# Optimization experiments

Measured on AMD Instinct MI355X. Metric: run time of the kernel, lower is better.

The kernel has to match this reference:

```python
import jax, jax.numpy as jnp
import numpy as np
from jax import lax

C = 32    # feats_channels
CT = 16   # transform_channels
B, D, H, W = 1, 16, 16, 32  # N = D*H*W = 8192


def _bcast(v):
    return v[None, :, None, None, None]


def conv1(x, w):
    # 1x1x1 Conv3d, no bias: w [O, I], x [b, I, d, h, w]
    return jnp.einsum('oi,bidhw->bodhw', w, x)


def cbr(x, w, s, b):
    # Conv1x1x1 + inference BatchNorm (folded to scale s / bias b) + ReLU
    return jax.nn.relu(conv1(x, w) * _bcast(s) + _bcast(b))


def setup_inputs() -> dict:
    key = jax.random.key(0)
    ks = jax.random.split(key, 16)

    def wmat(k, shape, scale=0.05):
        return jax.random.normal(k, shape, jnp.float32) * scale

    def bn(k, n):
        k1, k2 = jax.random.split(k)
        s = 1.0 + 0.05 * jax.random.normal(k1, (n,), jnp.float32)
        b = 0.05 * jax.random.normal(k2, (n,), jnp.float32)
        return s, b

    inp = {'x': jax.random.normal(ks[0], (B, C, D, H, W), jnp.float32)}
    # query_project: 2 convs (C->CT, CT->CT), each conv+BN+ReLU
    inp['wq1'] = wmat(ks[1], (CT, C));  inp['sq1'], inp['bq1'] = bn(ks[2], CT)
    inp['wq2'] = wmat(ks[3], (CT, CT)); inp['sq2'], inp['bq2'] = bn(ks[4], CT)
    # key_project: 2 convs (2C->CT, CT->CT)
    inp['wk1'] = wmat(ks[5], (CT, 2 * C)); inp['sk1'], inp['bk1'] = bn(ks[6], CT)
    inp['wk2'] = wmat(ks[7], (CT, CT));    inp['sk2'], inp['bk2'] = bn(ks[8], CT)
    # value_project: 1 conv (2C->CT) + BN + ReLU
    inp['wv'] = wmat(ks[9], (CT, 2 * C)); inp['sv'], inp['bv'] = bn(ks[10], CT)
    # out_project: 1 conv (CT->C) + BN + ReLU
    inp['wo'] = wmat(ks[11], (C, CT)); inp['so'], inp['bo'] = bn(ks[12], C)
    # bottleneck: Conv3d(2C->C, k=3, pad=1, no bias) + BN + LeakyReLU(0.1)
    inp['wbot'] = wmat(ks[13], (C, 2 * C, 3, 3, 3), 0.02)
    inp['sbot'], inp['bbot'] = bn(ks[14], C)
    return inp


def reference(x, wq1, sq1, bq1, wq2, sq2, bq2,
              wk1, sk1, bk1, wk2, sk2, bk2,
              wv, sv, bv, wo, so, bo, wbot, sbot, bbot):
    b, c, d, h, w = x.shape
    # AdaptiveAvgPool2d((1,1)) on (b, c*d, h, w) = mean over (h, w) per (c,d);
    # bilinear upsample from 1x1 is a constant broadcast.
    xg = jnp.mean(x, axis=(3, 4), keepdims=True)
    key_feats = jnp.concatenate([jnp.broadcast_to(xg, x.shape), x], axis=1)  # [b, 2c, d, h, w]

    q = cbr(cbr(x, wq1, sq1, bq1), wq2, sq2, bq2)          # [b, CT, d, h, w]
    k = cbr(cbr(key_feats, wk1, sk1, bk1), wk2, sk2, bk2)  # [b, CT, d, h, w]
    v = cbr(key_feats, wv, sv, bv)                          # [b, CT, d, h, w]

    n = d * h * w
    q = q.reshape(b, CT, n).transpose(0, 2, 1)  # [b, N, CT]
    k = k.reshape(b, CT, n)                     # [b, CT, N]
    v = v.reshape(b, CT, n).transpose(0, 2, 1)  # [b, N, CT]

    sim = jnp.einsum('bnc,bcm->bnm', q, k) * (CT ** -0.5)   # [b, N, N]
    sim = jax.nn.softmax(sim, axis=-1)
    ctx = jnp.einsum('bnm,bmc->bnc', sim, v)                # [b, N, CT]
    ctx = ctx.transpose(0, 2, 1).reshape(b, CT, d, h, w)
    ctx = cbr(ctx, wo, so, bo)                              # [b, C, d, h, w]

    fused = jnp.concatenate([x, ctx], axis=1)               # [b, 2C, d, h, w]
    y = lax.conv_general_dilated(
        fused, wbot, window_strides=(1, 1, 1), padding='SAME',
        dimension_numbers=('NCDHW', 'OIDHW', 'NCDHW'))
    y = y * _bcast(sbot) + _bcast(bbot)
    return jnp.where(y > 0, y, 0.1 * y)  # LeakyReLU(0.1)
```

## Files before the change

### kernel.cpp

```cpp
#include <hip/hip_runtime.h>

typedef unsigned int u32;
typedef unsigned short u16;
typedef float f32x16 __attribute__((ext_vector_type(16)));
typedef __bf16 bf16x8 __attribute__((ext_vector_type(8)));
union BF8 { u32 w[4]; bf16x8 v; };

#define DEVI static __device__ __forceinline__
DEVI u32 pk_bf16(float lo, float hi) {
  u32 r;
  asm("v_cvt_pk_bf16_f32 %0, %1, %2" : "=v"(r) : "v"(lo), "v"(hi));
  return r;
}
DEVI u16 bf1(float x) { return (u16)(pk_bf16(x, 0.0f) & 0xffffu); }

#define WB_WREP  0
#define WB_QS    131072
#define WB_K     393216
#define WB_VT    655360
#define WB_FUS   917504

__global__ __launch_bounds__(256) void k_prep(
    const float* __restrict__ x,
    const float* __restrict__ wq1, const float* __restrict__ sq1, const float* __restrict__ bq1,
    const float* __restrict__ wq2, const float* __restrict__ sq2, const float* __restrict__ bq2,
    const float* __restrict__ wk1, const float* __restrict__ sk1, const float* __restrict__ bk1,
    const float* __restrict__ wk2, const float* __restrict__ sk2, const float* __restrict__ bk2,
    const float* __restrict__ wv,  const float* __restrict__ sv,  const float* __restrict__ bv,
    const float* __restrict__ wbot, const float* __restrict__ sbot,
    u16* __restrict__ qs, u16* __restrict__ kbm, u16* __restrict__ vt,
    u16* __restrict__ fus, u16* __restrict__ wrep) {
  const int tid = threadIdx.x;
  const int bid = blockIdx.x;
  if (bid >= 256) {
    const int rb = bid - 256;
#pragma unroll
    for (int e = 0; e < 8; ++e) {
      const int idx = rb * 2048 + tid * 8 + e;
      const int tap = idx >> 11, rem = idx & 2047, o = rem >> 6, i = rem & 63;
      wrep[idx] = bf1(wbot[(o * 64 + i) * 27 + tap] * sbot[o]);
    }
    return;
  }
  __shared__ float H[2][32][17];
  __shared__ float P8[32][8];
  __shared__ float xgs[32];
  const int n0 = bid << 5;
  const int d = n0 >> 9;
  {
    const int c = tid >> 3, part = tid & 7;
    const float4* xp = (const float4*)(x + (c << 13) + (d << 9));
    float s = 0.f;
#pragma unroll
    for (int i = 0; i < 16; ++i) {
      const float4 v4 = xp[part + (i << 3)];
      s += v4.x + v4.y + v4.z + v4.w;
    }
    P8[c][part] = s;
  }
  __syncthreads();
  if (tid < 32) {
    float s = 0.f;
#pragma unroll
    for (int j = 0; j < 8; ++j) s += P8[tid][j];
    xgs[tid] = s * (1.0f / 512.0f);
  }
  __syncthreads();
  const int nl = tid & 31, g = tid >> 5;
  const int n = n0 + nl;
  const int r0 = 2 * g, r1 = r0 + 1;
  float xr[32], xgv[32];
#pragma unroll
  for (int c = 0; c < 32; ++c) xr[c] = x[(c << 13) + n];
#pragma unroll
  for (int c = 0; c < 32; ++c) xgv[c] = xgs[c];

  const float4* wq1f = (const float4*)wq1;
  const float4* wk1f = (const float4*)wk1;
  const float4* wvf  = (const float4*)wv;
  float dq0 = 0.f, dq1 = 0.f, dk0 = 0.f, dk1 = 0.f, dv0 = 0.f, dv1 = 0.f;
#pragma unroll
  for (int c4 = 0; c4 < 8; ++c4) {
    const float4 wa = wq1f[r0 * 8 + c4], wb = wq1f[r1 * 8 + c4];
    dq0 += wa.x * xr[4*c4+0] + wa.y * xr[4*c4+1] + wa.z * xr[4*c4+2] + wa.w * xr[4*c4+3];
    dq1 += wb.x * xr[4*c4+0] + wb.y * xr[4*c4+1] + wb.z * xr[4*c4+2] + wb.w * xr[4*c4+3];
  }
#pragma unroll
  for (int c4 = 0; c4 < 8; ++c4) {
    const float4 ka = wk1f[r0 * 16 + c4], kb = wk1f[r1 * 16 + c4];
    dk0 += ka.x * xgv[4*c4+0] + ka.y * xgv[4*c4+1] + ka.z * xgv[4*c4+2] + ka.w * xgv[4*c4+3];
    dk1 += kb.x * xgv[4*c4+0] + kb.y * xgv[4*c4+1] + kb.z * xgv[4*c4+2] + kb.w * xgv[4*c4+3];
    const float4 va = wvf[r0 * 16 + c4], vb = wvf[r1 * 16 + c4];
    dv0 += va.x * xgv[4*c4+0] + va.y * xgv[4*c4+1] + va.z * xgv[4*c4+2] + va.w * xgv[4*c4+3];
    dv1 += vb.x * xgv[4*c4+0] + vb.y * xgv[4*c4+1] + vb.z * xgv[4*c4+2] + vb.w * xgv[4*c4+3];
  }
#pragma unroll
  for (int c4 = 0; c4 < 8; ++c4) {
    const float4 ka = wk1f[r0 * 16 + 8 + c4], kb = wk1f[r1 * 16 + 8 + c4];
    dk0 += ka.x * xr[4*c4+0] + ka.y * xr[4*c4+1] + ka.z * xr[4*c4+2] + ka.w * xr[4*c4+3];
    dk1 += kb.x * xr[4*c4+0] + kb.y * xr[4*c4+1] + kb.z * xr[4*c4+2] + kb.w * xr[4*c4+3];
    const float4 va = wvf[r0 * 16 + 8 + c4], vb = wvf[r1 * 16 + 8 + c4];
    dv0 += va.x * xr[4*c4+0] + va.y * xr[4*c4+1] + va.z * xr[4*c4+2] + va.w * xr[4*c4+3];
    dv1 += vb.x * xr[4*c4+0] + vb.y * xr[4*c4+1] + vb.z * xr[4*c4+2] + vb.w * xr[4*c4+3];
  }
  const float hq0 = fmaxf(dq0 * sq1[r0] + bq1[r0], 0.f);
  const float hq1 = fmaxf(dq1 * sq1[r1] + bq1[r1], 0.f);
  const float hk0 = fmaxf(dk0 * sk1[r0] + bk1[r0], 0.f);
  const float hk1 = fmaxf(dk1 * sk1[r1] + bk1[r1], 0.f);
  const float hv0 = fmaxf(dv0 * sv[r0] + bv[r0], 0.f);
  const float hv1 = fmaxf(dv1 * sv[r1] + bv[r1], 0.f);
  H[0][nl][r0] = hq0; H[0][nl][r1] = hq1;
  H[1][nl][r0] = hk0; H[1][nl][r1] = hk1;
  vt[(r0 << 13) + n] = bf1(hv0);
  vt[(r1 << 13) + n] = bf1(hv1);
  const int c0 = g << 2;
  *(u32*)(fus + (n << 6) + c0)     = pk_bf16(xr[c0],     xr[c0 + 1]);
  *(u32*)(fus + (n << 6) + c0 + 2) = pk_bf16(xr[c0 + 2], xr[c0 + 3]);
  __syncthreads();

  float eq0 = 0.f, eq1 = 0.f, ek0 = 0.f, ek1 = 0.f;
#pragma unroll
  for (int j = 0; j < 16; ++j) {
    const float hq = H[0][nl][j], hk = H[1][nl][j];
    eq0 += wq2[r0 * 16 + j] * hq;
    eq1 += wq2[r1 * 16 + j] * hq;
    ek0 += wk2[r0 * 16 + j] * hk;
    ek1 += wk2[r1 * 16 + j] * hk;
  }
  const float SC = 0.36067376022224085f;
  const float q0 = fmaxf(eq0 * (sq2[r0] * SC) + bq2[r0] * SC, 0.f);
  const float q1 = fmaxf(eq1 * (sq2[r1] * SC) + bq2[r1] * SC, 0.f);
  const float k0 = fmaxf(ek0 * sk2[r0] + bk2[r0], 0.f);
  const float k1 = fmaxf(ek1 * sk2[r1] + bk2[r1], 0.f);
  *(u32*)(qs  + (n << 4) + r0) = pk_bf16(q0, q1);
  *(u32*)(kbm + (n << 4) + r0) = pk_bf16(k0, k1);
}

__global__ __launch_bounds__(1024) void k_attn(
    const u16* __restrict__ qs, const u16* __restrict__ kbm, const u16* __restrict__ vt,
    const float* __restrict__ wo, const float* __restrict__ so, const float* __restrict__ bo,
    u16* __restrict__ fus) {
  __shared__ float R[16][32][17];
  const int tid = threadIdx.x;
  const int w = tid >> 6, lane = tid & 63;
  const int l31 = lane & 31, h = lane >> 5;
  const int qb = blockIdx.x;

  const bf16x8 qf = *(const bf16x8*)(qs + (((qb << 5) + l31) << 4) + (h << 3));
  f32x16 acc_a, acc_b, z;
#pragma unroll
  for (int i = 0; i < 16; ++i) { acc_a[i] = 0.f; acc_b[i] = 0.f; z[i] = 0.f; }

  const u32 fill = (l31 == 16) ? 0x3F803F80u : 0u;
  const int kb0 = w << 9;
  const bool vlane = (l31 < 16);
  const u16* vrow = vt + (l31 << 13) + (h << 3);

  bf16x8 kf_c = *(const bf16x8*)(kbm + ((kb0 + l31) << 4) + (h << 3));
  BF8 V1c, V2c;
#pragma unroll
  for (int j2 = 0; j2 < 4; ++j2) { V1c.w[j2] = fill; V2c.w[j2] = fill; }
  if (vlane) {
    V1c.v = *(const bf16x8*)(vrow + kb0);
    V2c.v = *(const bf16x8*)(vrow + kb0 + 16);
  }

#pragma unroll
  for (int t = 0; t < 16; ++t) {
    const bf16x8 kf = kf_c;
    const BF8 V1 = V1c, V2 = V2c;
    if (t < 15) {
      const int kbn = kb0 + ((t + 1) << 5);
      kf_c = *(const bf16x8*)(kbm + ((kbn + l31) << 4) + (h << 3));
      if (vlane) {
        V1c.v = *(const bf16x8*)(vrow + kbn);
        V2c.v = *(const bf16x8*)(vrow + kbn + 16);
      }
    }
    const f32x16 st = __builtin_amdgcn_mfma_f32_32x32x16_bf16(kf, qf, z, 0, 0, 0);
    float pe[16];
#pragma unroll
    for (int r = 0; r < 16; ++r) pe[r] = __builtin_amdgcn_exp2f(st[r]);
    u32 a0 = pk_bf16(pe[0],  pe[1]),  a1 = pk_bf16(pe[2],  pe[3]);
    u32 a2 = pk_bf16(pe[4],  pe[5]),  a3 = pk_bf16(pe[6],  pe[7]);
    u32 b0 = pk_bf16(pe[8],  pe[9]),  b1 = pk_bf16(pe[10], pe[11]);
    u32 b2 = pk_bf16(pe[12], pe[13]), b3 = pk_bf16(pe[14], pe[15]);
    asm("v_permlane32_swap_b32 %0, %1" : "+v"(a0), "+v"(a2));
    asm("v_permlane32_swap_b32 %0, %1" : "+v"(a1), "+v"(a3));
    asm("v_permlane32_swap_b32 %0, %1" : "+v"(b0), "+v"(b2));
    asm("v_permlane32_swap_b32 %0, %1" : "+v"(b1), "+v"(b3));
    BF8 A1, A2;
    A1.w[0] = a0; A1.w[1] = a1; A1.w[2] = a2; A1.w[3] = a3;
    A2.w[0] = b0; A2.w[1] = b1; A2.w[2] = b2; A2.w[3] = b3;
    __builtin_amdgcn_s_setprio(1);
    acc_a = __builtin_amdgcn_mfma_f32_32x32x16_bf16(A1.v, V1.v, acc_a, 0, 0, 0);
    acc_b = __builtin_amdgcn_mfma_f32_32x32x16_bf16(A2.v, V2.v, acc_b, 0, 0, 0);
    __builtin_amdgcn_s_setprio(0);
  }
  if (l31 < 17) {
#pragma unroll
    for (int r = 0; r < 16; ++r) {
      const int row = (r & 3) + ((r >> 2) << 3) + (h << 2);
      R[w][row][l31] = acc_a[r] + acc_b[r];
    }
  }
  __syncthreads();
  float* Rf = &R[0][0][0];
  if (tid < 544) {
    float s0 = 0.f;
#pragma unroll
    for (int w2 = 0; w2 < 16; ++w2) s0 += Rf[w2 * 544 + tid];
    Rf[tid] = s0;
  }
  __syncthreads();
  if (tid < 512) {
    const int row = tid >> 4;
    const int o0 = (tid & 15) << 1, o1 = o0 + 1;
    const float inv = 1.0f / Rf[row * 17 + 16];
    float d0 = 0.f, d1 = 0.f;
#pragma unroll
    for (int c = 0; c < 16; ++c) {
      const float cv = Rf[row * 17 + c];
      d0 += wo[o0 * 16 + c] * cv;
      d1 += wo[o1 * 16 + c] * cv;
    }
    const float y0 = fmaxf(bo[o0] + so[o0] * d0 * inv, 0.f);
    const float y1 = fmaxf(bo[o1] + so[o1] * d1 * inv, 0.f);
    *(u32*)(fus + (((qb << 5) + row) << 6) + 32 + o0) = pk_bf16(y0, y1);
  }
}

__global__ __launch_bounds__(512) void k_conv(
    const u16* __restrict__ fus, const u16* __restrict__ wrep,
    const float* __restrict__ bbot, float* __restrict__ out) {
  __shared__ float R8[8][1024];
  const int tid = threadIdx.x;
  const int wv = tid >> 6, lane = tid & 63;
  const int l31 = lane & 31, h = lane >> 5;
  const int n0 = blockIdx.x << 5;
  const int dz = n0 >> 9, hy = (n0 >> 5) & 15;
  f32x16 acc0, acc1;
#pragma unroll
  for (int i = 0; i < 16; ++i) { acc0[i] = 0.f; acc1[i] = 0.f; }
  const int ulo = (wv * 54) >> 3, uhi = ((wv + 1) * 54) >> 3;

  const u16* bp_c; const u16* wp_c; bool ok_c;
  {
    const int tap = ulo >> 1, ch = (ulo & 1) << 1;
    const int dd = tap / 9 - 1, dh = (tap / 3) % 3 - 1, dw = tap % 3 - 1;
    ok_c = ((unsigned)(dz + dd) < 16u) & ((unsigned)(hy + dh) < 16u) &
           ((unsigned)(l31 + dw) < 32u);
    const int nn = n0 + dd * 512 + dh * 32 + dw + l31;
    bp_c = fus + (nn << 6) + (ch << 4) + (h << 3);
    wp_c = wrep + ((tap * 32 + l31) << 6) + (ch << 4) + (h << 3);
  }
  BF8 B0c, B1c;
  B0c.w[0] = B0c.w[1] = B0c.w[2] = B0c.w[3] = 0u;
  B1c.w[0] = B1c.w[1] = B1c.w[2] = B1c.w[3] = 0u;
  if (ok_c) { B0c.v = *(const bf16x8*)bp_c; B1c.v = *(const bf16x8*)(bp_c + 16); }

  for (int u = ulo; u < uhi; ++u) {
    const BF8 B0 = B0c, B1 = B1c;
    const u16* wp = wp_c;
    if (u + 1 < uhi) {
      const int un = u + 1;
      const int tap = un >> 1, ch = (un & 1) << 1;
      const int dd = tap / 9 - 1, dh = (tap / 3) % 3 - 1, dw = tap % 3 - 1;
      const bool ok = ((unsigned)(dz + dd) < 16u) & ((unsigned)(hy + dh) < 16u) &
                      ((unsigned)(l31 + dw) < 32u);
      const int nn = n0 + dd * 512 + dh * 32 + dw + l31;
      const u16* bp = fus + (nn << 6) + (ch << 4) + (h << 3);
      wp_c = wrep + ((tap * 32 + l31) << 6) + (ch << 4) + (h << 3);
      B0c.w[0] = B0c.w[1] = B0c.w[2] = B0c.w[3] = 0u;
      B1c.w[0] = B1c.w[1] = B1c.w[2] = B1c.w[3] = 0u;
      if (ok) { B0c.v = *(const bf16x8*)bp; B1c.v = *(const bf16x8*)(bp + 16); }
    }
    const bf16x8 af0 = *(const bf16x8*)wp;
    const bf16x8 af1 = *(const bf16x8*)(wp + 16);
    __builtin_amdgcn_s_setprio(1);
    acc0 = __builtin_amdgcn_mfma_f32_32x32x16_bf16(af0, B0.v, acc0, 0, 0, 0);
    acc1 = __builtin_amdgcn_mfma_f32_32x32x16_bf16(af1, B1.v, acc1, 0, 0, 0);
    __builtin_amdgcn_s_setprio(0);
  }
#pragma unroll
  for (int r = 0; r < 16; ++r) {
    const int row = (r & 3) + ((r >> 2) << 3) + (h << 2);
    R8[wv][(row << 5) + l31] = acc0[r] + acc1[r];
  }
  __syncthreads();
#pragma unroll
  for (int k2 = 0; k2 < 2; ++k2) {
    const int e = tid + (k2 << 9);
    const int row = e >> 5;
    float yv = bbot[row];
#pragma unroll
    for (int w2 = 0; w2 < 8; ++w2) yv += R8[w2][e];
    out[(row << 13) + n0 + (e & 31)] = yv > 0.f ? yv : 0.1f * yv;
  }
}

extern "C" void kernel_launch(void* const* d_in, const int* in_sizes, int n_in,
                              void* d_out, int out_size, void* d_ws, size_t ws_size,
                              hipStream_t stream) {
  const float* x    = (const float*)d_in[0];
  const float* wq1  = (const float*)d_in[1];
  const float* sq1  = (const float*)d_in[2];
  const float* bq1  = (const float*)d_in[3];
  const float* wq2  = (const float*)d_in[4];
  const float* sq2  = (const float*)d_in[5];
  const float* bq2  = (const float*)d_in[6];
  const float* wk1  = (const float*)d_in[7];
  const float* sk1  = (const float*)d_in[8];
  const float* bk1  = (const float*)d_in[9];
  const float* wk2  = (const float*)d_in[10];
  const float* sk2  = (const float*)d_in[11];
  const float* bk2  = (const float*)d_in[12];
  const float* wv   = (const float*)d_in[13];
  const float* sv   = (const float*)d_in[14];
  const float* bv   = (const float*)d_in[15];
  const float* wo   = (const float*)d_in[16];
  const float* so   = (const float*)d_in[17];
  const float* bo   = (const float*)d_in[18];
  const float* wbot = (const float*)d_in[19];
  const float* sbot = (const float*)d_in[20];
  const float* bbot = (const float*)d_in[21];
  (void)in_sizes; (void)n_in; (void)out_size; (void)ws_size;

  char* wsb = (char*)d_ws;
  u16* wrep = (u16*)(wsb + WB_WREP);
  u16* qs   = (u16*)(wsb + WB_QS);
  u16* kbm  = (u16*)(wsb + WB_K);
  u16* vt   = (u16*)(wsb + WB_VT);
  u16* fus  = (u16*)(wsb + WB_FUS);
  float* out = (float*)d_out;

  k_prep<<<283, 256, 0, stream>>>(x, wq1, sq1, bq1, wq2, sq2, bq2,
                                  wk1, sk1, bk1, wk2, sk2, bk2,
                                  wv, sv, bv, wbot, sbot,
                                  qs, kbm, vt, fus, wrep);
  k_attn<<<256, 1024, 0, stream>>>(qs, kbm, vt, wo, so, bo, fus);
  k_conv<<<256, 512, 0, stream>>>(fus, wrep, bbot, out);
}
```

Before: 35.90 us.

## Double prep block width and tile V as per-block contiguous chunks

```diff
diff --git a/kernel.cpp b/kernel.cpp
--- a/kernel.cpp
+++ b/kernel.cpp
@@ -17,10 +17,10 @@
 #define WB_WREP  0
 #define WB_QS    131072
 #define WB_K     393216
-#define WB_VT    655360
+#define WB_VTS   655360
 #define WB_FUS   917504
 
-__global__ __launch_bounds__(256) void k_prep(
+__global__ __launch_bounds__(512) void k_prep(
     const float* __restrict__ x,
     const float* __restrict__ wq1, const float* __restrict__ sq1, const float* __restrict__ bq1,
     const float* __restrict__ wq2, const float* __restrict__ sq2, const float* __restrict__ bq2,
@@ -28,7 +28,7 @@
     const float* __restrict__ wk2, const float* __restrict__ sk2, const float* __restrict__ bk2,
     const float* __restrict__ wv,  const float* __restrict__ sv,  const float* __restrict__ bv,
     const float* __restrict__ wbot, const float* __restrict__ sbot,
-    u16* __restrict__ qs, u16* __restrict__ kbm, u16* __restrict__ vt,
+    u16* __restrict__ qs, u16* __restrict__ kbm, u16* __restrict__ vts,
     u16* __restrict__ fus, u16* __restrict__ wrep) {
   const int tid = threadIdx.x;
   const int bid = blockIdx.x;
@@ -36,108 +36,103 @@
     const int rb = bid - 256;
 #pragma unroll
     for (int e = 0; e < 8; ++e) {
-      const int idx = rb * 2048 + tid * 8 + e;
-      const int tap = idx >> 11, rem = idx & 2047, o = rem >> 6, i = rem & 63;
-      wrep[idx] = bf1(wbot[(o * 64 + i) * 27 + tap] * sbot[o]);
+      const int idx = rb * 4096 + tid * 8 + e;
+      if (idx < 55296) {
+        const int tap = idx >> 11, rem = idx & 2047, o = rem >> 6, i = rem & 63;
+        wrep[idx] = bf1(wbot[(o * 64 + i) * 27 + tap] * sbot[o]);
+      }
     }
     return;
   }
-  __shared__ float H[2][32][17];
-  __shared__ float P8[32][8];
-  __shared__ float xgs[32];
+  __shared__ float SH[1664];
   const int n0 = bid << 5;
   const int d = n0 >> 9;
   {
-    const int c = tid >> 3, part = tid & 7;
+    const int c = tid >> 4, part = tid & 15;
     const float4* xp = (const float4*)(x + (c << 13) + (d << 9));
     float s = 0.f;
 #pragma unroll
-    for (int i = 0; i < 16; ++i) {
-      const float4 v4 = xp[part + (i << 3)];
+    for (int i = 0; i < 8; ++i) {
+      const float4 v4 = xp[part + (i << 4)];
       s += v4.x + v4.y + v4.z + v4.w;
     }
-    P8[c][part] = s;
+    SH[1088 + (c << 4) + part] = s;
   }
   __syncthreads();
   if (tid < 32) {
     float s = 0.f;
 #pragma unroll
-    for (int j = 0; j < 8; ++j) s += P8[tid][j];
-    xgs[tid] = s * (1.0f / 512.0f);
+    for (int j = 0; j < 16; ++j) s += SH[1088 + (tid << 4) + j];
+    SH[1600 + tid] = s * (1.0f / 512.0f);
   }
   __syncthreads();
   const int nl = tid & 31, g = tid >> 5;
   const int n = n0 + nl;
-  const int r0 = 2 * g, r1 = r0 + 1;
-  float xr[32], xgv[32];
-#pragma unroll
-  for (int c = 0; c < 32; ++c) xr[c] = x[(c << 13) + n];
-#pragma unroll
-  for (int c = 0; c < 32; ++c) xgv[c] = xgs[c];
-
-  const float4* wq1f = (const float4*)wq1;
-  const float4* wk1f = (const float4*)wk1;
-  const float4* wvf  = (const float4*)wv;
-  float dq0 = 0.f, dq1 = 0.f, dk0 = 0.f, dk1 = 0.f, dv0 = 0.f, dv1 = 0.f;
-#pragma unroll
-  for (int c4 = 0; c4 < 8; ++c4) {
-    const float4 wa = wq1f[r0 * 8 + c4], wb = wq1f[r1 * 8 + c4];
-    dq0 += wa.x * xr[4*c4+0] + wa.y * xr[4*c4+1] + wa.z * xr[4*c4+2] + wa.w * xr[4*c4+3];
-    dq1 += wb.x * xr[4*c4+0] + wb.y * xr[4*c4+1] + wb.z * xr[4*c4+2] + wb.w * xr[4*c4+3];
-  }
-#pragma unroll
-  for (int c4 = 0; c4 < 8; ++c4) {
-    const float4 ka = wk1f[r0 * 16 + c4], kb = wk1f[r1 * 16 + c4];
-    dk0 += ka.x * xgv[4*c4+0] + ka.y * xgv[4*c4+1] + ka.z * xgv[4*c4+2] + ka.w * xgv[4*c4+3];
-    dk1 += kb.x * xgv[4*c4+0] + kb.y * xgv[4*c4+1] + kb.z * xgv[4*c4+2] + kb.w * xgv[4*c4+3];
-    const float4 va = wvf[r0 * 16 + c4], vb = wvf[r1 * 16 + c4];
-    dv0 += va.x * xgv[4*c4+0] + va.y * xgv[4*c4+1] + va.z * xgv[4*c4+2] + va.w * xgv[4*c4+3];
-    dv1 += vb.x * xgv[4*c4+0] + vb.y * xgv[4*c4+1] + vb.z * xgv[4*c4+2] + vb.w * xgv[4*c4+3];
-  }
-#pragma unroll
-  for (int c4 = 0; c4 < 8; ++c4) {
-    const float4 ka = wk1f[r0 * 16 + 8 + c4], kb = wk1f[r1 * 16 + 8 + c4];
-    dk0 += ka.x * xr[4*c4+0] + ka.y * xr[4*c4+1] + ka.z * xr[4*c4+2] + ka.w * xr[4*c4+3];
-    dk1 += kb.x * xr[4*c4+0] + kb.y * xr[4*c4+1] + kb.z * xr[4*c4+2] + kb.w * xr[4*c4+3];
-    const float4 va = wvf[r0 * 16 + 8 + c4], vb = wvf[r1 * 16 + 8 + c4];
-    dv0 += va.x * xr[4*c4+0] + va.y * xr[4*c4+1] + va.z * xr[4*c4+2] + va.w * xr[4*c4+3];
-    dv1 += vb.x * xr[4*c4+0] + vb.y * xr[4*c4+1] + vb.z * xr[4*c4+2] + vb.w * xr[4*c4+3];
-  }
-  const float hq0 = fmaxf(dq0 * sq1[r0] + bq1[r0], 0.f);
-  const float hq1 = fmaxf(dq1 * sq1[r1] + bq1[r1], 0.f);
-  const float hk0 = fmaxf(dk0 * sk1[r0] + bk1[r0], 0.f);
-  const float hk1 = fmaxf(dk1 * sk1[r1] + bk1[r1], 0.f);
-  const float hv0 = fmaxf(dv0 * sv[r0] + bv[r0], 0.f);
-  const float hv1 = fmaxf(dv1 * sv[r1] + bv[r1], 0.f);
-  H[0][nl][r0] = hq0; H[0][nl][r1] = hq1;
-  H[1][nl][r0] = hk0; H[1][nl][r1] = hk1;
-  vt[(r0 << 13) + n] = bf1(hv0);
-  vt[(r1 << 13) + n] = bf1(hv1);
-  const int c0 = g << 2;
-  *(u32*)(fus + (n << 6) + c0)     = pk_bf16(xr[c0],     xr[c0 + 1]);
-  *(u32*)(fus + (n << 6) + c0 + 2) = pk_bf16(xr[c0 + 2], xr[c0 + 3]);
-  __syncthreads();
-
-  float eq0 = 0.f, eq1 = 0.f, ek0 = 0.f, ek1 = 0.f;
-#pragma unroll
-  for (int j = 0; j < 16; ++j) {
-    const float hq = H[0][nl][j], hk = H[1][nl][j];
-    eq0 += wq2[r0 * 16 + j] * hq;
-    eq1 += wq2[r1 * 16 + j] * hq;
-    ek0 += wk2[r0 * 16 + j] * hk;
-    ek1 += wk2[r1 * 16 + j] * hk;
-  }
-  const float SC = 0.36067376022224085f;
-  const float q0 = fmaxf(eq0 * (sq2[r0] * SC) + bq2[r0] * SC, 0.f);
-  const float q1 = fmaxf(eq1 * (sq2[r1] * SC) + bq2[r1] * SC, 0.f);
-  const float k0 = fmaxf(ek0 * sk2[r0] + bk2[r0], 0.f);
-  const float k1 = fmaxf(ek1 * sk2[r1] + bk2[r1], 0.f);
-  *(u32*)(qs  + (n << 4) + r0) = pk_bf16(q0, q1);
-  *(u32*)(kbm + (n << 4) + r0) = pk_bf16(k0, k1);
+  {
+    float xr[32], xgv[32];
+#pragma unroll
+    for (int c = 0; c < 32; ++c) xr[c] = x[(c << 13) + n];
+#pragma unroll
+    for (int c = 0; c < 32; ++c) xgv[c] = SH[1600 + c];
+
+    const float4* wq1f = (const float4*)wq1;
+    const float4* wk1f = (const float4*)wk1;
+    const float4* wvf  = (const float4*)wv;
+    float dq = 0.f, dk = 0.f, dv = 0.f;
+#pragma unroll
+    for (int c4 = 0; c4 < 8; ++c4) {
+      const float4 wa = wq1f[g * 8 + c4];
+      dq += wa.x * xr[4*c4+0] + wa.y * xr[4*c4+1] + wa.z * xr[4*c4+2] + wa.w * xr[4*c4+3];
+    }
+#pragma unroll
+    for (int c4 = 0; c4 < 8; ++c4) {
+      const float4 ka = wk1f[g * 16 + c4];
+      dk += ka.x * xgv[4*c4+0] + ka.y * xgv[4*c4+1] + ka.z * xgv[4*c4+2] + ka.w * xgv[4*c4+3];
+      const float4 va = wvf[g * 16 + c4];
+      dv += va.x * xgv[4*c4+0] + va.y * xgv[4*c4+1] + va.z * xgv[4*c4+2] + va.w * xgv[4*c4+3];
+    }
+#pragma unroll
+    for (int c4 = 0; c4 < 8; ++c4) {
+      const float4 ka = wk1f[g * 16 + 8 + c4];
+      dk += ka.x * xr[4*c4+0] + ka.y * xr[4*c4+1] + ka.z * xr[4*c4+2] + ka.w * xr[4*c4+3];
+      const float4 va = wvf[g * 16 + 8 + c4];
+      dv += va.x * xr[4*c4+0] + va.y * xr[4*c4+1] + va.z * xr[4*c4+2] + va.w * xr[4*c4+3];
+    }
+    const float hq = fmaxf(dq * sq1[g] + bq1[g], 0.f);
+    const float hk = fmaxf(dk * sk1[g] + bk1[g], 0.f);
+    const float hv = fmaxf(dv * sv[g] + bv[g], 0.f);
+    SH[nl * 17 + g] = hq;
+    SH[544 + nl * 17 + g] = hk;
+    vts[(bid << 9) + (g << 5) + nl] = bf1(hv);
+    const int c0 = g << 1;
+    *(u32*)(fus + (n << 6) + c0) = pk_bf16(xr[c0], xr[c0 + 1]);
+  }
+  __syncthreads();
+  if (tid < 256) {
+    const int nl2 = tid & 31, g2 = tid >> 5;
+    const int n2 = n0 + nl2;
+    const int r0 = 2 * g2, r1 = r0 + 1;
+    float eq0 = 0.f, eq1 = 0.f, ek0 = 0.f, ek1 = 0.f;
+#pragma unroll
+    for (int j = 0; j < 16; ++j) {
+      const float hq = SH[nl2 * 17 + j], hk = SH[544 + nl2 * 17 + j];
+      eq0 += wq2[r0 * 16 + j] * hq;
+      eq1 += wq2[r1 * 16 + j] * hq;
+      ek0 += wk2[r0 * 16 + j] * hk;
+      ek1 += wk2[r1 * 16 + j] * hk;
+    }
+    const float SC = 0.36067376022224085f;
+    const float q0 = fmaxf(eq0 * (sq2[r0] * SC) + bq2[r0] * SC, 0.f);
+    const float q1 = fmaxf(eq1 * (sq2[r1] * SC) + bq2[r1] * SC, 0.f);
+    const float k0 = fmaxf(ek0 * sk2[r0] + bk2[r0], 0.f);
+    const float k1 = fmaxf(ek1 * sk2[r1] + bk2[r1], 0.f);
+    *(u32*)(qs  + (n2 << 4) + r0) = pk_bf16(q0, q1);
+    *(u32*)(kbm + (n2 << 4) + r0) = pk_bf16(k0, k1);
+  }
 }
 
 __global__ __launch_bounds__(1024) void k_attn(
-    const u16* __restrict__ qs, const u16* __restrict__ kbm, const u16* __restrict__ vt,
+    const u16* __restrict__ qs, const u16* __restrict__ kbm, const u16* __restrict__ vts,
     const float* __restrict__ wo, const float* __restrict__ so, const float* __restrict__ bo,
     u16* __restrict__ fus) {
   __shared__ float R[16][32][17];
@@ -153,16 +148,17 @@
 
   const u32 fill = (l31 == 16) ? 0x3F803F80u : 0u;
   const int kb0 = w << 9;
+  const int t0 = w << 4;
   const bool vlane = (l31 < 16);
-  const u16* vrow = vt + (l31 << 13) + (h << 3);
+  const u16* vbase = vts + (l31 << 5) + (h << 3);
 
   bf16x8 kf_c = *(const bf16x8*)(kbm + ((kb0 + l31) << 4) + (h << 3));
   BF8 V1c, V2c;
 #pragma unroll
   for (int j2 = 0; j2 < 4; ++j2) { V1c.w[j2] = fill; V2c.w[j2] = fill; }
   if (vlane) {
-    V1c.v = *(const bf16x8*)(vrow + kb0);
-    V2c.v = *(const bf16x8*)(vrow + kb0 + 16);
+    V1c.v = *(const bf16x8*)(vbase + (t0 << 9));
+    V2c.v = *(const bf16x8*)(vbase + (t0 << 9) + 16);
   }
 
 #pragma unroll
@@ -173,8 +169,9 @@
       const int kbn = kb0 + ((t + 1) << 5);
       kf_c = *(const bf16x8*)(kbm + ((kbn + l31) << 4) + (h << 3));
       if (vlane) {
-        V1c.v = *(const bf16x8*)(vrow + kbn);
-        V2c.v = *(const bf16x8*)(vrow + kbn + 16);
+        const u16* vp = vbase + ((t0 + t + 1) << 9);
+        V1c.v = *(const bf16x8*)vp;
+        V2c.v = *(const bf16x8*)(vp + 16);
       }
     }
     const f32x16 st = __builtin_amdgcn_mfma_f32_32x32x16_bf16(kf, qf, z, 0, 0, 0);
@@ -330,14 +327,14 @@
   u16* wrep = (u16*)(wsb + WB_WREP);
   u16* qs   = (u16*)(wsb + WB_QS);
   u16* kbm  = (u16*)(wsb + WB_K);
-  u16* vt   = (u16*)(wsb + WB_VT);
+  u16* vts  = (u16*)(wsb + WB_VTS);
   u16* fus  = (u16*)(wsb + WB_FUS);
   float* out = (float*)d_out;
 
-  k_prep<<<283, 256, 0, stream>>>(x, wq1, sq1, bq1, wq2, sq2, bq2,
+  k_prep<<<270, 512, 0, stream>>>(x, wq1, sq1, bq1, wq2, sq2, bq2,
                                   wk1, sk1, bk1, wk2, sk2, bk2,
                                   wv, sv, bv, wbot, sbot,
-                                  qs, kbm, vt, fus, wrep);
-  k_attn<<<256, 1024, 0, stream>>>(qs, kbm, vt, wo, so, bo, fus);
+                                  qs, kbm, vts, fus, wrep);
+  k_attn<<<256, 1024, 0, stream>>>(qs, kbm, vts, wo, so, bo, fus);
   k_conv<<<256, 512, 0, stream>>>(fus, wrep, bbot, out);
 }
```

After: 35.58 us. About the same (-0.9%).
